# Kernel tuning notes

Hardware: AMD Instinct MI355X
Metric: run time of the kernel (lower is better)

The kernel has to match this reference:

```python
import jax, jax.numpy as jnp
import numpy as np
from jax import lax

D = 1024
K = 3
LN_EPS = 1e-5


def setup_inputs() -> dict:
    key = jax.random.key(0)
    ks = jax.random.split(key, 8)
    B, T = 8, 4096
    x = jax.random.normal(ks[0], (B, T, D), dtype=jnp.float32)
    s = 1.0 / np.sqrt(D)
    in_proj_w = jax.random.uniform(ks[1], (D, 2 * D), jnp.float32, -s, s)
    in_proj_b = jax.random.uniform(ks[2], (2 * D,), jnp.float32, -s, s)
    conv_w = jax.random.uniform(ks[3], (D, 1, K), jnp.float32, -1.0 / np.sqrt(K), 1.0 / np.sqrt(K))
    conv_b = jax.random.uniform(ks[4], (D,), jnp.float32, -1.0 / np.sqrt(K), 1.0 / np.sqrt(K))
    logit_a = jnp.zeros((D,), jnp.float32)
    ssm_b = jnp.full((D,), 0.1, jnp.float32)
    ssm_c = jnp.ones((D,), jnp.float32)
    ssm_d = jnp.zeros((D,), jnp.float32)
    out_proj_w = jax.random.uniform(ks[5], (D, D), jnp.float32, -s, s)
    out_proj_b = jax.random.uniform(ks[6], (D,), jnp.float32, -s, s)
    ln_w = jnp.ones((D,), jnp.float32)
    ln_b = jnp.zeros((D,), jnp.float32)
    return {"x": x, "in_proj_w": in_proj_w, "in_proj_b": in_proj_b,
            "conv_w": conv_w, "conv_b": conv_b, "logit_a": logit_a,
            "ssm_b": ssm_b, "ssm_c": ssm_c, "ssm_d": ssm_d,
            "out_proj_w": out_proj_w, "out_proj_b": out_proj_b,
            "ln_w": ln_w, "ln_b": ln_b}


def _dwconv(v, conv_w, conv_b):
    # v: (B, T, D) -> depthwise conv1d, kernel K, 'same' padding
    vt = jnp.transpose(v, (0, 2, 1))  # (B, D, T)
    out = lax.conv_general_dilated(
        vt, conv_w, window_strides=(1,), padding=[(K // 2, K // 2)],
        dimension_numbers=("NCH", "OIH", "NCH"), feature_group_count=D)
    out = out + conv_b[None, :, None]
    return jnp.transpose(out, (0, 2, 1))  # (B, T, D)


def reference(x, in_proj_w, in_proj_b, conv_w, conv_b, logit_a,
              ssm_b, ssm_c, ssm_d, out_proj_w, out_proj_b, ln_w, ln_b):
    B, T, _ = x.shape
    residual = x
    uv = x @ in_proj_w + in_proj_b                      # (B, T, 2D)
    u, v = uv[..., :D], uv[..., D:]
    v = jax.nn.silu(v)
    v_local = _dwconv(v, conv_w, conv_b)                # (B, T, D)

    a = jax.nn.sigmoid(logit_a).astype(v_local.dtype)
    # diagonal LTI scan: h_t = a*h_{t-1} + b*u_t ; y_t = c*h_t + d*u_t
    def step(h, vt):
        h = a * h + ssm_b * vt
        return h, ssm_c * h + ssm_d * vt
    h0 = jnp.zeros((B, D), v_local.dtype)
    _, y_seq = lax.scan(step, h0, jnp.transpose(v_local, (1, 0, 2)))
    y_seq = jnp.transpose(y_seq, (1, 0, 2))             # (B, T, D)

    out = u * jax.nn.silu(y_seq)
    out = out @ out_proj_w + out_proj_b                 # dropout: eval mode (identity)
    h = out + residual
    mu = jnp.mean(h, axis=-1, keepdims=True)
    var = jnp.mean(jnp.square(h - mu), axis=-1, keepdims=True)
    return (h - mu) * lax.rsqrt(var + LN_EPS) * ln_w + ln_b
```

## Files before the change

### kernel.cpp

```cpp
#include <hip/hip_runtime.h>
#include <cstdint>
#include <cstddef>

#define D_DIM   1024
#define TWO_D   2048
#define B_DIM   8
#define T_DIM   4096
#define BT_DIM  (B_DIM*T_DIM)
#define LN_EPS  1e-5f
#define NCHUNK  128
#define CLEN    (T_DIM/NCHUNK)

typedef __attribute__((ext_vector_type(8))) short bf16x8;
typedef __attribute__((ext_vector_type(4))) float f32x4;

__device__ __forceinline__ float bf2f(unsigned short u){
  union { unsigned int i; float f; } c; c.i = ((unsigned int)u) << 16; return c.f;
}
__device__ __forceinline__ unsigned short f2bf(float f){
  union { float f; unsigned int i; } c; c.f = f;
  unsigned int x = c.i;
  return (unsigned short)((x + 0x7fffu + ((x >> 16) & 1u)) >> 16);
}
__device__ __forceinline__ float sigmoidf_(float x){ return 1.f/(1.f+__expf(-x)); }
__device__ __forceinline__ float siluf_(float x){ return x/(1.f+__expf(-x)); }


__global__ void cvt_f32_bf16(const float* __restrict__ in, unsigned short* __restrict__ out, int n){
  int i = (blockIdx.x*blockDim.x + threadIdx.x)*4;
  const int stride = gridDim.x*blockDim.x*4;
  for (; i + 3 < n; i += stride){
    float4 f = *(const float4*)(in + i);
    ushort4 o; o.x=f2bf(f.x); o.y=f2bf(f.y); o.z=f2bf(f.z); o.w=f2bf(f.w);
    *(ushort4*)(out + i) = o;
  }
}

__global__ __launch_bounds__(256) void cvt_transpose(
    const float* __restrict__ W, unsigned short* __restrict__ Wt,
    int rows, int cols)
{
  __shared__ float tile[32][33];
  const int tx = threadIdx.x & 31;
  const int ty = threadIdx.x >> 5;
  const int tpc = cols >> 5;
  const int bc = blockIdx.x % tpc;
  const int br = blockIdx.x / tpc;
  const int gc = bc*32 + tx;
  const int gr = br*32;
#pragma unroll
  for (int i = 0; i < 32; i += 8)
    tile[ty + i][tx] = W[(size_t)(gr + ty + i)*cols + gc];
  __syncthreads();
#pragma unroll
  for (int i = 0; i < 32; i += 8)
    Wt[(size_t)(bc*32 + ty + i)*rows + gr + tx] = f2bf(tile[tx][ty + i]);
}

template<int EPI>
__global__ __launch_bounds__(512, 2) void gemm256(
    const unsigned short* __restrict__ A,
    const unsigned short* __restrict__ Bt,
    const float* __restrict__ bias,
    const float* __restrict__ resid,
    unsigned short* __restrict__ outU,
    unsigned short* __restrict__ outV,
    const int K, const int nbn)
{
  __shared__ __align__(16) unsigned short sA[2][2][8192];
  __shared__ __align__(16) unsigned short sB[2][2][8192];

#define BARRIER()   __builtin_amdgcn_s_barrier()
#define FENCE()     __builtin_amdgcn_sched_barrier(0)
#define WAIT_VM4()  do { asm volatile("s_waitcnt vmcnt(4)"); FENCE(); } while(0)
#define WAIT_VM0()  do { asm volatile("s_waitcnt vmcnt(0)"); FENCE(); } while(0)

  const int tid  = threadIdx.x;
  const int lane = tid & 63;
  const int wv   = tid >> 6;
  const int wr   = wv >> 2;
  const int wc   = wv & 3;
  const int fr   = lane & 15;
  const int fq   = lane >> 4;

  const int nwg = gridDim.x;
  const int cpx = nwg >> 3;
  const int wg  = (blockIdx.x & 7) * cpx + (blockIdx.x >> 3);
  const int bm = wg / nbn, bn = wg % nbn;

  const unsigned short* Ag = A  + (size_t)bm * 256 * K;
  const unsigned short* Bg = Bt + (size_t)bn * 256 * K;

  const int r0  = tid >> 2;
  const int r1  = 128 + r0;
  const int c0  = tid & 3;
  const int cs0 = c0 ^ ((r0 >> 1) & 3);
  const int cs1 = c0 ^ ((r1 >> 1) & 3);
  const int ld0 = tid * 8;
  const int ld1 = (512 + tid) * 8;

#define STAGE(ARR, srcp, kofs)                                                           \
  do {                                                                                   \
    __builtin_amdgcn_global_load_lds(                                                    \
      (const __attribute__((address_space(1))) void*)((srcp) + (size_t)r0*K + (kofs) + cs0*8), \
      (__attribute__((address_space(3))) void*)(&(ARR)[ld0]), 16, 0, 0);                 \
    __builtin_amdgcn_global_load_lds(                                                    \
      (const __attribute__((address_space(1))) void*)((srcp) + (size_t)r1*K + (kofs) + cs1*8), \
      (__attribute__((address_space(3))) void*)(&(ARR)[ld1]), 16, 0, 0);                 \
  } while(0)

  const int swz  = fq ^ ((fr >> 1) & 3);
  const int offA = (wr*128 + fr) * 32 + swz * 8;
  const int offB = (wc*64  + fr) * 32 + swz * 8;

  f32x4 acc[8][4];
#pragma unroll
  for (int i = 0; i < 8; ++i)
#pragma unroll
    for (int j = 0; j < 4; ++j) acc[i][j] = {0.f,0.f,0.f,0.f};

  bf16x8 afr[4], bfr[4];

#define PHASE(PAR, KH, MH, STAGE_STMT, TAIL_WAIT)                          \
  do {                                                                     \
    _Pragma("unroll")                                                      \
    for (int m2 = 0; m2 < 4; ++m2)                                         \
      afr[m2] = *(const bf16x8*)(&sA[PAR][KH][offA + ((MH)*4+m2)*512]);    \
    if ((MH) == 0) {                                                       \
      _Pragma("unroll")                                                    \
      for (int n2 = 0; n2 < 4; ++n2)                                       \
        bfr[n2] = *(const bf16x8*)(&sB[PAR][KH][offB + n2*512]);           \
    }                                                                      \
    STAGE_STMT;                                                            \
    __builtin_amdgcn_s_setprio(1);                                         \
    _Pragma("unroll")                                                      \
    for (int n2 = 0; n2 < 4; ++n2)                                         \
      _Pragma("unroll")                                                    \
      for (int m2 = 0; m2 < 4; ++m2)                                       \
        acc[(MH)*4+m2][n2] = __builtin_amdgcn_mfma_f32_16x16x32_bf16(      \
            afr[m2], bfr[n2], acc[(MH)*4+m2][n2], 0, 0, 0);                \
    __builtin_amdgcn_s_setprio(0);                                         \
    TAIL_WAIT;                                                             \
    BARRIER();                                                             \
  } while(0)

  const int npairs = K >> 7;

  STAGE(sA[0][0], Ag, 0);
  STAGE(sB[0][0], Bg, 0);
  STAGE(sA[0][1], Ag, 32);
  STAGE(sB[0][1], Bg, 32);
  WAIT_VM4();
  BARRIER();

  for (int i = 0; i < npairs - 1; ++i){
    const int kbO = ((i << 1) + 1) << 6;
    const int kbE = ((i << 1) + 2) << 6;
    PHASE(0, 0, 0, STAGE(sA[1][0], Ag, kbO),      );
    PHASE(0, 0, 1, STAGE(sB[1][0], Bg, kbO),      WAIT_VM4());
    PHASE(0, 1, 0, STAGE(sA[1][1], Ag, kbO + 32), );
    PHASE(0, 1, 1, STAGE(sB[1][1], Bg, kbO + 32), WAIT_VM4());
    PHASE(1, 0, 0, STAGE(sA[0][0], Ag, kbE),      );
    PHASE(1, 0, 1, STAGE(sB[0][0], Bg, kbE),      WAIT_VM4());
    PHASE(1, 1, 0, STAGE(sA[0][1], Ag, kbE + 32), );
    PHASE(1, 1, 1, STAGE(sB[0][1], Bg, kbE + 32), WAIT_VM4());
  }
  PHASE(0, 0, 0, STAGE(sA[1][0], Ag, K - 64), );
  PHASE(0, 0, 1, STAGE(sB[1][0], Bg, K - 64), WAIT_VM4());
  PHASE(0, 1, 0, STAGE(sA[1][1], Ag, K - 32), );
  PHASE(0, 1, 1, STAGE(sB[1][1], Bg, K - 32), WAIT_VM4());
  PHASE(1, 0, 0, , );
  PHASE(1, 0, 1, , WAIT_VM0());
  PHASE(1, 1, 0, , );
  PHASE(1, 1, 1, , );

  const int nb = bn*256 + wc*64;
  const int mb = bm*256 + wr*128;
  float bsv[4];
#pragma unroll
  for (int ni = 0; ni < 4; ++ni) bsv[ni] = bias[nb + ni*16 + fr];

  if (EPI == 0){
    const bool isV = (nb >= D_DIM);
    unsigned short* dst = isV ? (outV + (nb - D_DIM)) : (outU + nb);
#pragma unroll
    for (int mi = 0; mi < 8; ++mi){
#pragma unroll
      for (int j = 0; j < 4; ++j){
        const int m = mb + mi*16 + fq*4 + j;
        unsigned short* row = dst + (size_t)m*D_DIM + fr;
#pragma unroll
        for (int ni = 0; ni < 4; ++ni){
          float cv = acc[mi][ni][j] + bsv[ni];
          row[ni*16] = f2bf(isV ? siluf_(cv) : cv);
        }
      }
    }
  } else {
#pragma unroll
    for (int mi = 0; mi < 8; ++mi){
#pragma unroll
      for (int j = 0; j < 4; ++j){
        const int m = mb + mi*16 + fq*4 + j;
        const float* rrow = resid + (size_t)m*D_DIM + nb + fr;
        unsigned short* orow = outU + (size_t)m*D_DIM + nb + fr;
#pragma unroll
        for (int ni = 0; ni < 4; ++ni)
          orow[ni*16] = f2bf(acc[mi][ni][j] + bsv[ni] + rrow[ni*16]);
      }
    }
  }
#undef PHASE
#undef STAGE
#undef BARRIER
#undef FENCE
#undef WAIT_VM4
#undef WAIT_VM0
}

__global__ __launch_bounds__(256) void scan_a(
    const unsigned short* __restrict__ v,
    const float* __restrict__ conv_w, const float* __restrict__ conv_b,
    const float* __restrict__ logit_a, const float* __restrict__ ssm_b,
    float* __restrict__ hend)
{
  const int b = blockIdx.x / NCHUNK;
  const int c = blockIdx.x % NCHUNK;
  const int d0 = threadIdx.x * 4;
  const int t0 = c * CLEN;
  const unsigned short* vb = v + (size_t)b * T_DIM * D_DIM;

  float w0[4], w1[4], w2[4], av[4], bv[4], cb[4];
#pragma unroll
  for (int i=0;i<4;i++){
    w0[i] = conv_w[(d0+i)*3+0];
    w1[i] = conv_w[(d0+i)*3+1];
    w2[i] = conv_w[(d0+i)*3+2];
    cb[i] = conv_b[d0+i];
    av[i] = sigmoidf_(logit_a[d0+i]);
    bv[i] = ssm_b[d0+i];
  }
  float vm1[4], v0[4], h[4] = {0.f,0.f,0.f,0.f};
  if (t0 == 0){
#pragma unroll
    for (int i=0;i<4;i++) vm1[i]=0.f;
  } else {
    ushort4 u = *(const ushort4*)(vb + (size_t)(t0-1)*D_DIM + d0);
    vm1[0]=bf2f(u.x); vm1[1]=bf2f(u.y); vm1[2]=bf2f(u.z); vm1[3]=bf2f(u.w);
  }
  {
    ushort4 u = *(const ushort4*)(vb + (size_t)t0*D_DIM + d0);
    v0[0]=bf2f(u.x); v0[1]=bf2f(u.y); v0[2]=bf2f(u.z); v0[3]=bf2f(u.w);
  }
#pragma unroll 8
  for (int t = t0; t < t0 + CLEN; ++t){
    float vp1[4];
    if (t + 1 < T_DIM){
      ushort4 u = *(const ushort4*)(vb + (size_t)(t+1)*D_DIM + d0);
      vp1[0]=bf2f(u.x); vp1[1]=bf2f(u.y); vp1[2]=bf2f(u.z); vp1[3]=bf2f(u.w);
    } else { vp1[0]=vp1[1]=vp1[2]=vp1[3]=0.f; }
#pragma unroll
    for (int i=0;i<4;i++){
      float vl = w0[i]*vm1[i] + w1[i]*v0[i] + w2[i]*vp1[i] + cb[i];
      h[i] = av[i]*h[i] + bv[i]*vl;
      vm1[i]=v0[i]; v0[i]=vp1[i];
    }
  }
  float* he = hend + ((size_t)b*NCHUNK + c)*D_DIM + d0;
#pragma unroll
  for (int i=0;i<4;i++) he[i] = h[i];
}

__global__ void scan_fix(const float* __restrict__ hend, const float* __restrict__ logit_a,
                         float* __restrict__ hinit)
{
  int idx = blockIdx.x*blockDim.x + threadIdx.x;
  if (idx >= B_DIM*D_DIM) return;
  const int b = idx / D_DIM, d = idx % D_DIM;
  const float a  = sigmoidf_(logit_a[d]);
  const float aL = __powf(a, (float)CLEN);
  const float* hep = hend  + (size_t)b*NCHUNK*D_DIM + d;
  float*       hip = hinit + (size_t)b*NCHUNK*D_DIM + d;
  float h = 0.f;
  for (int cb = 0; cb < NCHUNK; cb += 8){
    float buf[8];
#pragma unroll
    for (int j = 0; j < 8; ++j)
      buf[j] = hep[(size_t)(cb + j)*D_DIM];
#pragma unroll
    for (int j = 0; j < 8; ++j){
      hip[(size_t)(cb + j)*D_DIM] = h;
      h = aL*h + buf[j];
    }
  }
}

__global__ __launch_bounds__(256) void scan_c(
    const unsigned short* __restrict__ v,
    const unsigned short* __restrict__ ubuf,
    const float* __restrict__ conv_w, const float* __restrict__ conv_b,
    const float* __restrict__ logit_a, const float* __restrict__ ssm_b,
    const float* __restrict__ ssm_c, const float* __restrict__ ssm_d,
    const float* __restrict__ hinit,
    unsigned short* __restrict__ gated)
{
  const int b = blockIdx.x / NCHUNK;
  const int c = blockIdx.x % NCHUNK;
  const int d0 = threadIdx.x * 4;
  const int t0 = c * CLEN;
  const unsigned short* vb = v    + (size_t)b * T_DIM * D_DIM;
  const unsigned short* ub = ubuf + (size_t)b * T_DIM * D_DIM;
  unsigned short* gb       = gated+ (size_t)b * T_DIM * D_DIM;

  float w0[4], w1[4], w2[4], av[4], bv[4], cb[4], scv[4], sdv[4], h[4];
#pragma unroll
  for (int i=0;i<4;i++){
    w0[i] = conv_w[(d0+i)*3+0];
    w1[i] = conv_w[(d0+i)*3+1];
    w2[i] = conv_w[(d0+i)*3+2];
    cb[i] = conv_b[d0+i];
    av[i] = sigmoidf_(logit_a[d0+i]);
    bv[i] = ssm_b[d0+i];
    scv[i] = ssm_c[d0+i];
    sdv[i] = ssm_d[d0+i];
    h[i] = hinit[((size_t)b*NCHUNK + c)*D_DIM + d0 + i];
  }
  float vm1[4], v0[4];
  if (t0 == 0){
#pragma unroll
    for (int i=0;i<4;i++) vm1[i]=0.f;
  } else {
    ushort4 u = *(const ushort4*)(vb + (size_t)(t0-1)*D_DIM + d0);
    vm1[0]=bf2f(u.x); vm1[1]=bf2f(u.y); vm1[2]=bf2f(u.z); vm1[3]=bf2f(u.w);
  }
  {
    ushort4 u = *(const ushort4*)(vb + (size_t)t0*D_DIM + d0);
    v0[0]=bf2f(u.x); v0[1]=bf2f(u.y); v0[2]=bf2f(u.z); v0[3]=bf2f(u.w);
  }
#pragma unroll 8
  for (int t = t0; t < t0 + CLEN; ++t){
    float vp1[4];
    if (t + 1 < T_DIM){
      ushort4 u = *(const ushort4*)(vb + (size_t)(t+1)*D_DIM + d0);
      vp1[0]=bf2f(u.x); vp1[1]=bf2f(u.y); vp1[2]=bf2f(u.z); vp1[3]=bf2f(u.w);
    } else { vp1[0]=vp1[1]=vp1[2]=vp1[3]=0.f; }
    ushort4 uu = *(const ushort4*)(ub + (size_t)t*D_DIM + d0);
    float uf[4] = { bf2f(uu.x), bf2f(uu.y), bf2f(uu.z), bf2f(uu.w) };
    ushort4 go;
    unsigned short gtmp[4];
#pragma unroll
    for (int i=0;i<4;i++){
      float vl = w0[i]*vm1[i] + w1[i]*v0[i] + w2[i]*vp1[i] + cb[i];
      h[i] = av[i]*h[i] + bv[i]*vl;
      float y = scv[i]*h[i] + sdv[i]*vl;
      gtmp[i] = f2bf(uf[i] * siluf_(y));
      vm1[i]=v0[i]; v0[i]=vp1[i];
    }
    go.x=gtmp[0]; go.y=gtmp[1]; go.z=gtmp[2]; go.w=gtmp[3];
    *(ushort4*)(gb + (size_t)t*D_DIM + d0) = go;
  }
}

__global__ __launch_bounds__(256) void ln_kernel(
    const unsigned short* __restrict__ hb, float* __restrict__ out,
    const float* __restrict__ lw, const float* __restrict__ lb)
{
  __shared__ float rs[4], rq[4];
  const int row = blockIdx.x;
  const int tid = threadIdx.x;
  const unsigned short* p = hb + (size_t)row * D_DIM;
  ushort4 u = *(const ushort4*)(p + tid*4);
  float x0 = bf2f(u.x), x1 = bf2f(u.y), x2 = bf2f(u.z), x3 = bf2f(u.w);
  float s = x0 + x1 + x2 + x3;
  float q = x0*x0 + x1*x1 + x2*x2 + x3*x3;
#pragma unroll
  for (int off = 32; off > 0; off >>= 1){
    s += __shfl_down(s, off, 64);
    q += __shfl_down(q, off, 64);
  }
  const int wv = tid >> 6;
  if ((tid & 63) == 0){ rs[wv] = s; rq[wv] = q; }
  __syncthreads();
  const float ts = rs[0]+rs[1]+rs[2]+rs[3];
  const float tq = rq[0]+rq[1]+rq[2]+rq[3];
  const float mu  = ts * (1.f/(float)D_DIM);
  const float var = tq * (1.f/(float)D_DIM) - mu*mu;
  const float inv = rsqrtf(var + LN_EPS);
  const float4 w4 = *(const float4*)(lw + tid*4);
  const float4 b4 = *(const float4*)(lb + tid*4);
  float4 o;
  o.x = (x0-mu)*inv*w4.x + b4.x;
  o.y = (x1-mu)*inv*w4.y + b4.y;
  o.z = (x2-mu)*inv*w4.z + b4.z;
  o.w = (x3-mu)*inv*w4.w + b4.w;
  *(float4*)(out + (size_t)row*D_DIM + tid*4) = o;
}

extern "C" void kernel_launch(void* const* d_in, const int* in_sizes, int n_in,
                              void* d_out, int out_size, void* d_ws, size_t ws_size,
                              hipStream_t stream)
{
  const float* x     = (const float*)d_in[0];
  const float* w1    = (const float*)d_in[1];
  const float* b1    = (const float*)d_in[2];
  const float* convw = (const float*)d_in[3];
  const float* convb = (const float*)d_in[4];
  const float* la    = (const float*)d_in[5];
  const float* sb    = (const float*)d_in[6];
  const float* sc    = (const float*)d_in[7];
  const float* sd    = (const float*)d_in[8];
  const float* w2    = (const float*)d_in[9];
  const float* b2    = (const float*)d_in[10];
  const float* lw    = (const float*)d_in[11];
  const float* lb    = (const float*)d_in[12];
  float* out = (float*)d_out;

  char* ws = (char*)d_ws;
  unsigned short* xb    = (unsigned short*)(ws + 0);
  unsigned short* ubf   = (unsigned short*)(ws + 67108864);
  unsigned short* vbf   = (unsigned short*)(ws + 134217728);
  unsigned short* w1t   = (unsigned short*)(ws + 201326592);
  unsigned short* w2t   = (unsigned short*)(ws + 205520896);
  float*          hend  = (float*)(ws + 207618048);
  float*          hinit = (float*)(ws + 211812352);

  cvt_f32_bf16<<<2048, 256, 0, stream>>>(x, xb, BT_DIM*D_DIM);
  cvt_transpose<<<(D_DIM/32)*(TWO_D/32), 256, 0, stream>>>(w1, w1t, D_DIM, TWO_D);
  cvt_transpose<<<(D_DIM/32)*(D_DIM/32), 256, 0, stream>>>(w2, w2t, D_DIM, D_DIM);

  gemm256<0><<<dim3((BT_DIM/256)*(TWO_D/256)), 512, 0, stream>>>(
      xb, w1t, b1, nullptr, ubf, vbf, D_DIM, TWO_D/256);

  scan_a<<<B_DIM*NCHUNK, 256, 0, stream>>>(vbf, convw, convb, la, sb, hend);
  scan_fix<<<(B_DIM*D_DIM + 255)/256, 256, 0, stream>>>(hend, la, hinit);
  scan_c<<<B_DIM*NCHUNK, 256, 0, stream>>>(vbf, ubf, convw, convb, la, sb, sc, sd, hinit, xb);

  gemm256<1><<<dim3((BT_DIM/256)*(D_DIM/256)), 512, 0, stream>>>(
      xb, w2t, b2, x, ubf, nullptr, D_DIM, D_DIM/256);

  ln_kernel<<<BT_DIM, 256, 0, stream>>>(ubf, out, lw, lb);
}
```

Measured before the change: 392.1 us.

## Use 1024-thread workgroups in GEMM with 16 waves splitting the 256x256 tile

The GEMM kernel now launches 1024 threads (16 waves in a 4x4 grid) instead of 512, so each wave owns a 64x64 sub-tile rather than 128x64. Staging issues one global-to-LDS load per thread per array and the pipeline is reorganised into four phases per k-pair, with vmcnt waits adjusted to match. The intent is more waves per CU to hide latency and a smaller accumulator footprint per wave. In exchange, each wave re-reads B fragments from LDS every phase, the LDS-read-to-MFMA ratio rises, and only one workgroup can be resident per CU, so barrier stalls hit the whole CU.

Result: no change. 394.8 us (median of 4 runs) (+0.7%).

```diff
diff --git a/kernel.cpp b/kernel.cpp
--- a/kernel.cpp
+++ b/kernel.cpp
@@ -58,7 +58,7 @@
 }
 
 template<int EPI>
-__global__ __launch_bounds__(512, 2) void gemm256(
+__global__ __launch_bounds__(1024) void gemm256(
     const unsigned short* __restrict__ A,
     const unsigned short* __restrict__ Bt,
     const float* __restrict__ bias,
@@ -72,7 +72,7 @@
 
 #define BARRIER()   __builtin_amdgcn_s_barrier()
 #define FENCE()     __builtin_amdgcn_sched_barrier(0)
-#define WAIT_VM4()  do { asm volatile("s_waitcnt vmcnt(4)"); FENCE(); } while(0)
+#define WAIT_VM2()  do { asm volatile("s_waitcnt vmcnt(2)"); FENCE(); } while(0)
 #define WAIT_VM0()  do { asm volatile("s_waitcnt vmcnt(0)"); FENCE(); } while(0)
 
   const int tid  = threadIdx.x;
@@ -92,53 +92,43 @@
   const unsigned short* Bg = Bt + (size_t)bn * 256 * K;
 
   const int r0  = tid >> 2;
-  const int r1  = 128 + r0;
   const int c0  = tid & 3;
   const int cs0 = c0 ^ ((r0 >> 1) & 3);
-  const int cs1 = c0 ^ ((r1 >> 1) & 3);
   const int ld0 = tid * 8;
-  const int ld1 = (512 + tid) * 8;
 
 #define STAGE(ARR, srcp, kofs)                                                           \
-  do {                                                                                   \
-    __builtin_amdgcn_global_load_lds(                                                    \
+  __builtin_amdgcn_global_load_lds(                                                     \
       (const __attribute__((address_space(1))) void*)((srcp) + (size_t)r0*K + (kofs) + cs0*8), \
-      (__attribute__((address_space(3))) void*)(&(ARR)[ld0]), 16, 0, 0);                 \
-    __builtin_amdgcn_global_load_lds(                                                    \
-      (const __attribute__((address_space(1))) void*)((srcp) + (size_t)r1*K + (kofs) + cs1*8), \
-      (__attribute__((address_space(3))) void*)(&(ARR)[ld1]), 16, 0, 0);                 \
-  } while(0)
+      (__attribute__((address_space(3))) void*)(&(ARR)[ld0]), 16, 0, 0)
 
   const int swz  = fq ^ ((fr >> 1) & 3);
-  const int offA = (wr*128 + fr) * 32 + swz * 8;
-  const int offB = (wc*64  + fr) * 32 + swz * 8;
-
-  f32x4 acc[8][4];
-#pragma unroll
-  for (int i = 0; i < 8; ++i)
+  const int offA = (wr*64 + fr) * 32 + swz * 8;
+  const int offB = (wc*64 + fr) * 32 + swz * 8;
+
+  f32x4 acc[4][4];
+#pragma unroll
+  for (int i = 0; i < 4; ++i)
 #pragma unroll
     for (int j = 0; j < 4; ++j) acc[i][j] = {0.f,0.f,0.f,0.f};
 
   bf16x8 afr[4], bfr[4];
 
-#define PHASE(PAR, KH, MH, STAGE_STMT, TAIL_WAIT)                          \
+#define PHASE(PAR, KH, STAGE_STMT, TAIL_WAIT)                              \
   do {                                                                     \
     _Pragma("unroll")                                                      \
     for (int m2 = 0; m2 < 4; ++m2)                                         \
-      afr[m2] = *(const bf16x8*)(&sA[PAR][KH][offA + ((MH)*4+m2)*512]);    \
-    if ((MH) == 0) {                                                       \
-      _Pragma("unroll")                                                    \
-      for (int n2 = 0; n2 < 4; ++n2)                                       \
-        bfr[n2] = *(const bf16x8*)(&sB[PAR][KH][offB + n2*512]);           \
-    }                                                                      \
+      afr[m2] = *(const bf16x8*)(&sA[PAR][KH][offA + m2*512]);             \
+    _Pragma("unroll")                                                      \
+    for (int n2 = 0; n2 < 4; ++n2)                                         \
+      bfr[n2] = *(const bf16x8*)(&sB[PAR][KH][offB + n2*512]);             \
     STAGE_STMT;                                                            \
     __builtin_amdgcn_s_setprio(1);                                         \
     _Pragma("unroll")                                                      \
-    for (int n2 = 0; n2 < 4; ++n2)                                         \
+    for (int m2 = 0; m2 < 4; ++m2)                                         \
       _Pragma("unroll")                                                    \
-      for (int m2 = 0; m2 < 4; ++m2)                                       \
-        acc[(MH)*4+m2][n2] = __builtin_amdgcn_mfma_f32_16x16x32_bf16(      \
-            afr[m2], bfr[n2], acc[(MH)*4+m2][n2], 0, 0, 0);                \
+      for (int n2 = 0; n2 < 4; ++n2)                                       \
+        acc[m2][n2] = __builtin_amdgcn_mfma_f32_16x16x32_bf16(             \
+            afr[m2], bfr[n2], acc[m2][n2], 0, 0, 0);                       \
     __builtin_amdgcn_s_setprio(0);                                         \
     TAIL_WAIT;                                                             \
     BARRIER();                                                             \
@@ -150,32 +140,24 @@
   STAGE(sB[0][0], Bg, 0);
   STAGE(sA[0][1], Ag, 32);
   STAGE(sB[0][1], Bg, 32);
-  WAIT_VM4();
+  WAIT_VM2();
   BARRIER();
 
   for (int i = 0; i < npairs - 1; ++i){
     const int kbO = ((i << 1) + 1) << 6;
     const int kbE = ((i << 1) + 2) << 6;
-    PHASE(0, 0, 0, STAGE(sA[1][0], Ag, kbO),      );
-    PHASE(0, 0, 1, STAGE(sB[1][0], Bg, kbO),      WAIT_VM4());
-    PHASE(0, 1, 0, STAGE(sA[1][1], Ag, kbO + 32), );
-    PHASE(0, 1, 1, STAGE(sB[1][1], Bg, kbO + 32), WAIT_VM4());
-    PHASE(1, 0, 0, STAGE(sA[0][0], Ag, kbE),      );
-    PHASE(1, 0, 1, STAGE(sB[0][0], Bg, kbE),      WAIT_VM4());
-    PHASE(1, 1, 0, STAGE(sA[0][1], Ag, kbE + 32), );
-    PHASE(1, 1, 1, STAGE(sB[0][1], Bg, kbE + 32), WAIT_VM4());
-  }
-  PHASE(0, 0, 0, STAGE(sA[1][0], Ag, K - 64), );
-  PHASE(0, 0, 1, STAGE(sB[1][0], Bg, K - 64), WAIT_VM4());
-  PHASE(0, 1, 0, STAGE(sA[1][1], Ag, K - 32), );
-  PHASE(0, 1, 1, STAGE(sB[1][1], Bg, K - 32), WAIT_VM4());
-  PHASE(1, 0, 0, , );
-  PHASE(1, 0, 1, , WAIT_VM0());
-  PHASE(1, 1, 0, , );
-  PHASE(1, 1, 1, , );
+    PHASE(0, 0, { STAGE(sA[1][0], Ag, kbO);      STAGE(sB[1][0], Bg, kbO);      }, WAIT_VM2());
+    PHASE(0, 1, { STAGE(sA[1][1], Ag, kbO + 32); STAGE(sB[1][1], Bg, kbO + 32); }, WAIT_VM2());
+    PHASE(1, 0, { STAGE(sA[0][0], Ag, kbE);      STAGE(sB[0][0], Bg, kbE);      }, WAIT_VM2());
+    PHASE(1, 1, { STAGE(sA[0][1], Ag, kbE + 32); STAGE(sB[0][1], Bg, kbE + 32); }, WAIT_VM2());
+  }
+  PHASE(0, 0, { STAGE(sA[1][0], Ag, K - 64); STAGE(sB[1][0], Bg, K - 64); }, WAIT_VM2());
+  PHASE(0, 1, { STAGE(sA[1][1], Ag, K - 32); STAGE(sB[1][1], Bg, K - 32); }, WAIT_VM2());
+  PHASE(1, 0, , WAIT_VM0());
+  PHASE(1, 1, , );
 
   const int nb = bn*256 + wc*64;
-  const int mb = bm*256 + wr*128;
+  const int mb = bm*256 + wr*64;
   float bsv[4];
 #pragma unroll
   for (int ni = 0; ni < 4; ++ni) bsv[ni] = bias[nb + ni*16 + fr];
@@ -184,7 +166,7 @@
     const bool isV = (nb >= D_DIM);
     unsigned short* dst = isV ? (outV + (nb - D_DIM)) : (outU + nb);
 #pragma unroll
-    for (int mi = 0; mi < 8; ++mi){
+    for (int mi = 0; mi < 4; ++mi){
 #pragma unroll
       for (int j = 0; j < 4; ++j){
         const int m = mb + mi*16 + fq*4 + j;
@@ -198,7 +180,7 @@
     }
   } else {
 #pragma unroll
-    for (int mi = 0; mi < 8; ++mi){
+    for (int mi = 0; mi < 4; ++mi){
 #pragma unroll
       for (int j = 0; j < 4; ++j){
         const int m = mb + mi*16 + fq*4 + j;
@@ -214,7 +196,7 @@
 #undef STAGE
 #undef BARRIER
 #undef FENCE
-#undef WAIT_VM4
+#undef WAIT_VM2
 #undef WAIT_VM0
 }
 
@@ -428,14 +410,14 @@
   cvt_transpose<<<(D_DIM/32)*(TWO_D/32), 256, 0, stream>>>(w1, w1t, D_DIM, TWO_D);
   cvt_transpose<<<(D_DIM/32)*(D_DIM/32), 256, 0, stream>>>(w2, w2t, D_DIM, D_DIM);
 
-  gemm256<0><<<dim3((BT_DIM/256)*(TWO_D/256)), 512, 0, stream>>>(
+  gemm256<0><<<dim3((BT_DIM/256)*(TWO_D/256)), 1024, 0, stream>>>(
       xb, w1t, b1, nullptr, ubf, vbf, D_DIM, TWO_D/256);
 
   scan_a<<<B_DIM*NCHUNK, 256, 0, stream>>>(vbf, convw, convb, la, sb, hend);
   scan_fix<<<(B_DIM*D_DIM + 255)/256, 256, 0, stream>>>(hend, la, hinit);
   scan_c<<<B_DIM*NCHUNK, 256, 0, stream>>>(vbf, ubf, convw, convb, la, sb, sc, sd, hinit, xb);
 
-  gemm256<1><<<dim3((BT_DIM/256)*(D_DIM/256)), 512, 0, stream>>>(
+  gemm256<1><<<dim3((BT_DIM/256)*(D_DIM/256)), 1024, 0, stream>>>(
       xb, w2t, b2, x, ubf, nullptr, D_DIM, D_DIM/256);
 
   ln_kernel<<<BT_DIM, 256, 0, stream>>>(ubf, out, lw, lb);
```
